# Kernel optimization log

Hardware: AMD Instinct MI355X
Metric: run time of the kernel (lower is better)

Reference implementation:

```python
import jax, jax.numpy as jnp
import numpy as np

N_NODES = 50000
N_EDGES = 800000
IN_DIM = 128
HIDDEN = 32
HEADS = 4
OUT_DIM = 40
NEG_SLOPE = 0.2


def _segment_softmax(logits, seg, num_segments):
    # logits: [E, H], seg: [E] destination node ids
    m = jax.ops.segment_max(logits, seg, num_segments=num_segments)  # [N, H]
    e = jnp.exp(logits - m[seg])
    s = jax.ops.segment_sum(e, seg, num_segments=num_segments)  # [N, H]
    return e / s[seg]


def _gat_conv(x, src, dst, W, a_src, a_dst, b, heads, out_ch, concat):
    N = x.shape[0]
    h = (x @ W).reshape(N, heads, out_ch)  # [N, H, C]
    alpha_src = jnp.einsum('nhc,hc->nh', h, a_src)  # [N, H]
    alpha_dst = jnp.einsum('nhc,hc->nh', h, a_dst)  # [N, H]
    logits = jax.nn.leaky_relu(alpha_src[src] + alpha_dst[dst], NEG_SLOPE)  # [E, H]
    alpha = _segment_softmax(logits, dst, N)  # [E, H]
    msg = h[src] * alpha[:, :, None]  # [E, H, C]
    out = jax.ops.segment_sum(msg, dst, num_segments=N)  # [N, H, C]
    if concat:
        out = out.reshape(N, heads * out_ch)
    else:
        out = out.mean(axis=1)
    return out + b


def setup_inputs() -> dict:
    key = jax.random.key(0)
    ks = jax.random.split(key, 12)
    x = jax.random.normal(ks[0], (N_NODES, IN_DIM), dtype=jnp.float32)
    edge_index = jax.random.randint(ks[1], (2, N_EDGES), 0, N_NODES, dtype=jnp.int64 if jax.config.read('jax_enable_x64') else jnp.int32)
    s1 = 1.0 / np.sqrt(IN_DIM)
    W1 = jax.random.uniform(ks[2], (IN_DIM, HEADS * HIDDEN), jnp.float32, -s1, s1)
    att_src1 = jax.random.uniform(ks[3], (HEADS, HIDDEN), jnp.float32, -1, 1) / np.sqrt(HIDDEN)
    att_dst1 = jax.random.uniform(ks[4], (HEADS, HIDDEN), jnp.float32, -1, 1) / np.sqrt(HIDDEN)
    b1 = jnp.zeros((HEADS * HIDDEN,), jnp.float32)
    s2 = 1.0 / np.sqrt(HEADS * HIDDEN)
    W2 = jax.random.uniform(ks[5], (HEADS * HIDDEN, OUT_DIM), jnp.float32, -s2, s2)
    att_src2 = jax.random.uniform(ks[6], (1, OUT_DIM), jnp.float32, -1, 1) / np.sqrt(OUT_DIM)
    att_dst2 = jax.random.uniform(ks[7], (1, OUT_DIM), jnp.float32, -1, 1) / np.sqrt(OUT_DIM)
    b2 = jnp.zeros((OUT_DIM,), jnp.float32)
    return {
        'x': x, 'edge_index': edge_index,
        'W1': W1, 'att_src1': att_src1, 'att_dst1': att_dst1, 'b1': b1,
        'W2': W2, 'att_src2': att_src2, 'att_dst2': att_dst2, 'b2': b2,
    }


def reference(x, edge_index, W1, att_src1, att_dst1, b1, W2, att_src2, att_dst2, b2):
    N = x.shape[0]
    # PyG GATConv default add_self_loops=True
    loop = jnp.arange(N, dtype=edge_index.dtype)
    src = jnp.concatenate([edge_index[0], loop])
    dst = jnp.concatenate([edge_index[1], loop])
    # dropout(p=0.6) is identity in eval mode
    h = _gat_conv(x, src, dst, W1, att_src1, att_dst1, b1, HEADS, HIDDEN, concat=True)
    h = jax.nn.relu(h)
    out = _gat_conv(h, src, dst, W2, att_src2, att_dst2, b2, 1, OUT_DIM, concat=True)
    return out
```

## Files before the change

### kernel.cpp

```cpp
#include <hip/hip_runtime.h>
#include <hip/hip_bf16.h>
#include <math.h>

#define N_NODES 50000
#define N_EDGES 800000
#define E_TOT   850000
#define IN_DIM  128
#define HID     32
#define HEADS   4
#define D1      128
#define OUT_DIM 40
#define H2P     64
#define NEG_SLOPE 0.2f

#define SCAN_TILE 1024
#define SCAN_NB   ((N_NODES + SCAN_TILE - 1) / SCAN_TILE)
#define GEMM1_NB  ((N_NODES + 31) / 32)
#define CNT_NB    ((E_TOT + 255) / 256)

__global__ __launch_bounds__(256) void gemm1_count(
    const float* __restrict__ x, const float* __restrict__ W,
    const float* __restrict__ as_v, const float* __restrict__ ad_v,
    float* __restrict__ h1, float* __restrict__ asrc, float* __restrict__ adst,
    const int* __restrict__ ei, int* __restrict__ deg)
{
  __shared__ float xs[32][IN_DIM];
  const int t = threadIdx.x;
  if (blockIdx.x >= GEMM1_NB) {
    int e = (blockIdx.x - GEMM1_NB) * 256 + t;
    if (e < E_TOT) {
      int d = (e < N_EDGES) ? ei[N_EDGES + e] : e - N_EDGES;
      atomicAdd(deg + d, 1);
    }
    return;
  }
  const int nb = blockIdx.x * 32;
  for (int i = t; i < 32 * (IN_DIM / 4); i += 256) {
    int r = i >> 5, k4 = (i & 31) * 4;
    int n = nb + r;
    float4 v = (n < N_NODES) ? *reinterpret_cast<const float4*>(x + (size_t)n * IN_DIM + k4)
                             : make_float4(0.f, 0.f, 0.f, 0.f);
    *reinterpret_cast<float4*>(&xs[r][k4]) = v;
  }
  __syncthreads();
  const int ct = t & 31, col0 = ct * 4;
  const int rt = t >> 5, rbase = rt * 4;
  float acc[4][4];
#pragma unroll
  for (int r = 0; r < 4; ++r)
#pragma unroll
    for (int c = 0; c < 4; ++c) acc[r][c] = 0.f;

  for (int k = 0; k < IN_DIM; k += 4) {
    float4 xv[4];
#pragma unroll
    for (int r = 0; r < 4; ++r)
      xv[r] = *reinterpret_cast<const float4*>(&xs[rbase + r][k]);
    float4 wv[4];
#pragma unroll
    for (int kk = 0; kk < 4; ++kk)
      wv[kk] = *reinterpret_cast<const float4*>(W + (size_t)(k + kk) * D1 + col0);
#pragma unroll
    for (int r = 0; r < 4; ++r) {
      acc[r][0] += xv[r].x * wv[0].x + xv[r].y * wv[1].x + xv[r].z * wv[2].x + xv[r].w * wv[3].x;
      acc[r][1] += xv[r].x * wv[0].y + xv[r].y * wv[1].y + xv[r].z * wv[2].y + xv[r].w * wv[3].y;
      acc[r][2] += xv[r].x * wv[0].z + xv[r].y * wv[1].z + xv[r].z * wv[2].z + xv[r].w * wv[3].z;
      acc[r][3] += xv[r].x * wv[0].w + xv[r].y * wv[1].w + xv[r].z * wv[2].w + xv[r].w * wv[3].w;
    }
  }

  const int head = col0 >> 5;
  const int cc0  = col0 & 31;
  const float4 asv = *reinterpret_cast<const float4*>(as_v + head * HID + cc0);
  const float4 adv = *reinterpret_cast<const float4*>(ad_v + head * HID + cc0);
#pragma unroll
  for (int r = 0; r < 4; ++r) {
    int n = nb + rbase + r;
    bool ok = n < N_NODES;
    if (ok) {
      float4 o = make_float4(acc[r][0], acc[r][1], acc[r][2], acc[r][3]);
      *reinterpret_cast<float4*>(h1 + (size_t)n * D1 + col0) = o;
    }
    float cs = acc[r][0] * asv.x + acc[r][1] * asv.y + acc[r][2] * asv.z + acc[r][3] * asv.w;
    float cd = acc[r][0] * adv.x + acc[r][1] * adv.y + acc[r][2] * adv.z + acc[r][3] * adv.w;
#pragma unroll
    for (int off = 1; off < 8; off <<= 1) {
      cs += __shfl_xor(cs, off, 64);
      cd += __shfl_xor(cd, off, 64);
    }
    if ((ct & 7) == 0 && ok) {
      asrc[n * HEADS + head] = cs;
      adst[n * HEADS + head] = cd;
    }
  }
}

__global__ void zero_deg(int* __restrict__ deg)
{
  int i = blockIdx.x * blockDim.x + threadIdx.x;
  if (i < N_NODES) deg[i] = 0;
}

__global__ __launch_bounds__(256) void scan_p1(const int* __restrict__ deg,
                                               int* __restrict__ blocksum)
{
  int base = blockIdx.x * SCAN_TILE + threadIdx.x * 4;
  int s = 0;
#pragma unroll
  for (int i = 0; i < 4; ++i) {
    int idx = base + i;
    if (idx < N_NODES) s += deg[idx];
  }
#pragma unroll
  for (int off = 1; off < 64; off <<= 1) s += __shfl_xor(s, off, 64);
  __shared__ int ws[4];
  if ((threadIdx.x & 63) == 0) ws[threadIdx.x >> 6] = s;
  __syncthreads();
  if (threadIdx.x == 0) blocksum[blockIdx.x] = ws[0] + ws[1] + ws[2] + ws[3];
}

__global__ void scan_p2(const int* __restrict__ blocksum, int* __restrict__ blockoff,
                        int* __restrict__ row_off)
{
  int t = threadIdx.x;
  int v = (t < SCAN_NB) ? blocksum[t] : 0;
  int incl = v;
#pragma unroll
  for (int off = 1; off < 64; off <<= 1) {
    int u = __shfl_up(incl, off, 64);
    if (t >= off) incl += u;
  }
  if (t < SCAN_NB) blockoff[t] = incl - v;
  if (t == 0) row_off[N_NODES] = E_TOT;
}

__global__ __launch_bounds__(256) void scan_p3(const int* __restrict__ deg,
                                               const int* __restrict__ blockoff,
                                               int* __restrict__ row_off,
                                               int* __restrict__ cursor)
{
  const int t = threadIdx.x;
  const int lane = t & 63, wid = t >> 6;
  int base = blockIdx.x * SCAN_TILE + t * 4;
  int local[4]; int lsum = 0;
#pragma unroll
  for (int i = 0; i < 4; ++i) {
    int idx = base + i;
    local[i] = (idx < N_NODES) ? deg[idx] : 0;
    lsum += local[i];
  }
  int incl = lsum;
#pragma unroll
  for (int off = 1; off < 64; off <<= 1) {
    int u = __shfl_up(incl, off, 64);
    if (lane >= off) incl += u;
  }
  __shared__ int wtot[4];
  if (lane == 63) wtot[wid] = incl;
  __syncthreads();
  int wpre = 0;
  for (int w = 0; w < wid; ++w) wpre += wtot[w];
  int run = blockoff[blockIdx.x] + wpre + (incl - lsum);
#pragma unroll
  for (int i = 0; i < 4; ++i) {
    int idx = base + i;
    if (idx < N_NODES) { row_off[idx] = run; cursor[idx] = run; run += local[i]; }
  }
}

__global__ void scatter_csr(const int* __restrict__ ei, int* __restrict__ cursor,
                            int* __restrict__ csr_src)
{
  int e = blockIdx.x * blockDim.x + threadIdx.x;
  if (e >= E_TOT) return;
  int s, d;
  if (e < N_EDGES) { s = ei[e]; d = ei[N_EDGES + e]; }
  else             { s = d = e - N_EDGES; }
  int pos = atomicAdd(cursor + d, 1);
  csr_src[pos] = s;
}

__global__ __launch_bounds__(256) void agg1(
    const int* __restrict__ row_off, const int* __restrict__ csr_src,
    const float* __restrict__ asrc, const float* __restrict__ adst,
    const float* __restrict__ h1, const float* __restrict__ b1,
    float* __restrict__ lbuf, float* __restrict__ z)
{
  int n = blockIdx.x * 4 + (threadIdx.x >> 6);
  if (n >= N_NODES) return;
  const int lane = threadIdx.x & 63;
  const int start = row_off[n], end = row_off[n + 1];
  const int h = lane & 3;
  const float adst_h = adst[n * HEADS + h];
  float vmax = -1e30f;
  for (int i = start + (lane >> 2); i < end; i += 16)
    vmax = fmaxf(vmax, asrc[csr_src[i] * HEADS + h]);
#pragma unroll
  for (int off = 4; off < 64; off <<= 1)
    vmax = fmaxf(vmax, __shfl_xor(vmax, off, 64));
  float v = vmax + adst_h;
  const float mle = v > 0.f ? v : NEG_SLOPE * v;
  float ssum = 0.f;
  for (int i = start + (lane >> 2); i < end; i += 16) {
    float tv = asrc[csr_src[i] * HEADS + h] + adst_h;
    float le = tv > 0.f ? tv : NEG_SLOPE * tv;
    float e = __expf(le - mle);
    lbuf[(size_t)i * 4 + h] = e;
    ssum += e;
  }
#pragma unroll
  for (int off = 4; off < 64; off <<= 1)
    ssum += __shfl_xor(ssum, off, 64);
  const int hh = lane >> 4;
  const float inv = 1.f / __shfl(ssum, hh, 64);
  float2 acc = make_float2(0.f, 0.f);
  int i = start;
  for (; i + 4 <= end; i += 4) {
    int s0 = csr_src[i], s1 = csr_src[i + 1], s2 = csr_src[i + 2], s3 = csr_src[i + 3];
    float c0 = lbuf[(size_t)(i    ) * 4 + hh];
    float c1 = lbuf[(size_t)(i + 1) * 4 + hh];
    float c2 = lbuf[(size_t)(i + 2) * 4 + hh];
    float c3 = lbuf[(size_t)(i + 3) * 4 + hh];
    float2 v0 = *reinterpret_cast<const float2*>(h1 + (size_t)s0 * D1 + 2 * lane);
    float2 v1 = *reinterpret_cast<const float2*>(h1 + (size_t)s1 * D1 + 2 * lane);
    float2 v2 = *reinterpret_cast<const float2*>(h1 + (size_t)s2 * D1 + 2 * lane);
    float2 v3 = *reinterpret_cast<const float2*>(h1 + (size_t)s3 * D1 + 2 * lane);
    acc.x += c0 * v0.x + c1 * v1.x + c2 * v2.x + c3 * v3.x;
    acc.y += c0 * v0.y + c1 * v1.y + c2 * v2.y + c3 * v3.y;
  }
  for (; i < end; ++i) {
    int s = csr_src[i];
    float c = lbuf[(size_t)i * 4 + hh];
    float2 hv = *reinterpret_cast<const float2*>(h1 + (size_t)s * D1 + 2 * lane);
    acc.x += c * hv.x;
    acc.y += c * hv.y;
  }
  float2 bb = *reinterpret_cast<const float2*>(b1 + 2 * lane);
  float r0 = acc.x * inv + bb.x;
  float r1 = acc.y * inv + bb.y;
  float2 o = make_float2(r0 > 0.f ? r0 : 0.f, r1 > 0.f ? r1 : 0.f);
  *reinterpret_cast<float2*>(z + (size_t)n * D1 + 2 * lane) = o;
}

__global__ __launch_bounds__(256) void gemm2(
    const float* __restrict__ z, const float* __restrict__ W2,
    const float* __restrict__ as2, const float* __restrict__ ad2,
    float* __restrict__ h2p, float* __restrict__ asrc2, float* __restrict__ adst2)
{
  __shared__ float zs[32][IN_DIM];
  const int nb = blockIdx.x * 32;
  const int t  = threadIdx.x;
  for (int i = t; i < 32 * (IN_DIM / 4); i += 256) {
    int r = i >> 5, k4 = (i & 31) * 4;
    int n = nb + r;
    float4 v = (n < N_NODES) ? *reinterpret_cast<const float4*>(z + (size_t)n * IN_DIM + k4)
                             : make_float4(0.f, 0.f, 0.f, 0.f);
    *reinterpret_cast<float4*>(&zs[r][k4]) = v;
  }
  __syncthreads();
  const int col = t & 63;
  const int rbase = (t >> 6) * 8;
  const bool valid = col < OUT_DIM;
  const int colc = valid ? col : (OUT_DIM - 1);
  float acc[8];
#pragma unroll
  for (int r = 0; r < 8; ++r) acc[r] = 0.f;
  for (int k = 0; k < IN_DIM; ++k) {
    float w = W2[k * OUT_DIM + colc];
#pragma unroll
    for (int r = 0; r < 8; ++r) acc[r] += zs[rbase + r][k] * w;
  }
  const float a_s = valid ? as2[col] : 0.f;
  const float a_d = valid ? ad2[col] : 0.f;
#pragma unroll
  for (int r = 0; r < 8; ++r) {
    int n = nb + rbase + r;
    float cs = acc[r] * a_s, cd = acc[r] * a_d;
#pragma unroll
    for (int off = 32; off >= 1; off >>= 1) {
      cs += __shfl_xor(cs, off, 64);
      cd += __shfl_xor(cd, off, 64);
    }
    if (n < N_NODES) {
      if (valid) h2p[(size_t)n * H2P + col] = acc[r];
      if (col == 0) { asrc2[n] = cs; adst2[n] = cd; }
    }
  }
}

__global__ __launch_bounds__(256) void agg2(
    const int* __restrict__ row_off, const int* __restrict__ csr_src,
    const float* __restrict__ asrc, const float* __restrict__ adst,
    const float* __restrict__ h2p, const float* __restrict__ b2,
    float* __restrict__ lbuf, float* __restrict__ out)
{
  int n = blockIdx.x * 4 + (threadIdx.x >> 6);
  if (n >= N_NODES) return;
  const int lane = threadIdx.x & 63;
  const int start = row_off[n], end = row_off[n + 1];
  const float adstn = adst[n];
  float vmax = -1e30f;
  for (int i = start + lane; i < end; i += 64)
    vmax = fmaxf(vmax, asrc[csr_src[i]]);
#pragma unroll
  for (int off = 1; off < 64; off <<= 1)
    vmax = fmaxf(vmax, __shfl_xor(vmax, off, 64));
  float v = vmax + adstn;
  const float mle = v > 0.f ? v : NEG_SLOPE * v;
  float ssum = 0.f;
  for (int i = start + lane; i < end; i += 64) {
    float t = asrc[csr_src[i]] + adstn;
    float le = t > 0.f ? t : NEG_SLOPE * t;
    float e = __expf(le - mle);
    lbuf[i] = e;
    ssum += e;
  }
#pragma unroll
  for (int off = 1; off < 64; off <<= 1)
    ssum += __shfl_xor(ssum, off, 64);
  const float inv = 1.f / ssum;
  if (lane < OUT_DIM) {
    float acc = 0.f;
    int i = start;
    for (; i + 4 <= end; i += 4) {
      int s0 = csr_src[i], s1 = csr_src[i + 1], s2 = csr_src[i + 2], s3 = csr_src[i + 3];
      float c0 = lbuf[i], c1 = lbuf[i + 1], c2 = lbuf[i + 2], c3 = lbuf[i + 3];
      acc += c0 * h2p[(size_t)s0 * H2P + lane]
           + c1 * h2p[(size_t)s1 * H2P + lane]
           + c2 * h2p[(size_t)s2 * H2P + lane]
           + c3 * h2p[(size_t)s3 * H2P + lane];
    }
    for (; i < end; ++i)
      acc += lbuf[i] * h2p[(size_t)csr_src[i] * H2P + lane];
    out[(size_t)n * OUT_DIM + lane] = acc * inv + b2[lane];
  }
}

extern "C" void kernel_launch(void* const* d_in, const int* in_sizes, int n_in,
                              void* d_out, int out_size, void* d_ws, size_t ws_size,
                              hipStream_t stream)
{
  const float* x    = (const float*)d_in[0];
  const int*   ei   = (const int*)  d_in[1];
  const float* W1   = (const float*)d_in[2];
  const float* as1  = (const float*)d_in[3];
  const float* ad1  = (const float*)d_in[4];
  const float* b1   = (const float*)d_in[5];
  const float* W2   = (const float*)d_in[6];
  const float* as2  = (const float*)d_in[7];
  const float* ad2  = (const float*)d_in[8];
  const float* b2   = (const float*)d_in[9];
  float* out = (float*)d_out;

  float* ws = (float*)d_ws;
  float* h1    = ws +  0;
  float* h2p   = ws +  0;
  float* z     = ws +  6400000;
  float* asrc1 = ws + 12800000;
  float* adst1 = ws + 13000000;
  float* asrc2 = ws + 13200000;
  float* adst2 = ws + 13250000;
  int* deg     = (int*)(ws + 13300000);
  int* row_off = (int*)(ws + 13350000);
  int* cursor  = (int*)(ws + 13410000);
  int* csr_src = (int*)(ws + 13460000);
  int* blocksum= (int*)(ws + 14320000);
  int* blockoff= (int*)(ws + 14320100);
  float* lbuf  = ws + 14400000;

  const int B = 256;
  zero_deg<<<(N_NODES + B - 1) / B, B, 0, stream>>>(deg);
  gemm1_count<<<GEMM1_NB + CNT_NB, B, 0, stream>>>(x, W1, as1, ad1, h1, asrc1, adst1, ei, deg);
  scan_p1<<<SCAN_NB, B, 0, stream>>>(deg, blocksum);
  scan_p2<<<1, 64, 0, stream>>>(blocksum, blockoff, row_off);
  scan_p3<<<SCAN_NB, B, 0, stream>>>(deg, blockoff, row_off, cursor);
  scatter_csr<<<(E_TOT + B - 1) / B, B, 0, stream>>>(ei, cursor, csr_src);
  agg1<<<(N_NODES + 3) / 4, B, 0, stream>>>(row_off, csr_src, asrc1, adst1, h1, b1, lbuf, z);
  gemm2<<<(N_NODES + 31) / 32, B, 0, stream>>>(z, W2, as2, ad2, h2p, asrc2, adst2);
  agg2<<<(N_NODES + 3) / 4, B, 0, stream>>>(row_off, csr_src, asrc2, adst2, h2p, b2, lbuf, out);
}
```

Baseline: 366.2 us.

## Stage GEMM weights in shared memory with larger row tiles

gemm1 now processes 64 rows per block (8 per thread) and streams W through a double-buffered shared-memory tile, prefetching the next 8 rows of W into registers during compute. Previously every thread read W straight from global memory. gemm2 now loads a transposed, padded copy of W2 into shared memory so each thread can read float4 weights along k instead of scalar global loads. This cuts global and cache traffic for the weights, at the cost of more shared memory, more registers, and an extra barrier per k-step in gemm1. The GEMMs are only part of a larger pipeline dominated by edge gathers, so the overall effect is bounded.

```diff
diff --git a/kernel.cpp b/kernel.cpp
--- a/kernel.cpp
+++ b/kernel.cpp
@@ -15,8 +15,10 @@
 
 #define SCAN_TILE 1024
 #define SCAN_NB   ((N_NODES + SCAN_TILE - 1) / SCAN_TILE)
-#define GEMM1_NB  ((N_NODES + 31) / 32)
+#define G1_ROWS   64
+#define GEMM1_NB  ((N_NODES + G1_ROWS - 1) / G1_ROWS)
 #define CNT_NB    ((E_TOT + 255) / 256)
+#define W2T_LD    132
 
 __global__ __launch_bounds__(256) void gemm1_count(
     const float* __restrict__ x, const float* __restrict__ W,
@@ -24,7 +26,8 @@
     float* __restrict__ h1, float* __restrict__ asrc, float* __restrict__ adst,
     const int* __restrict__ ei, int* __restrict__ deg)
 {
-  __shared__ float xs[32][IN_DIM];
+  __shared__ float xs[G1_ROWS][IN_DIM];
+  __shared__ float wbuf[2][8 * D1];
   const int t = threadIdx.x;
   if (blockIdx.x >= GEMM1_NB) {
     int e = (blockIdx.x - GEMM1_NB) * 256 + t;
@@ -34,39 +37,53 @@
     }
     return;
   }
-  const int nb = blockIdx.x * 32;
-  for (int i = t; i < 32 * (IN_DIM / 4); i += 256) {
+  const int nb = blockIdx.x * G1_ROWS;
+  for (int i = t; i < G1_ROWS * (IN_DIM / 4); i += 256) {
     int r = i >> 5, k4 = (i & 31) * 4;
     int n = nb + r;
     float4 v = (n < N_NODES) ? *reinterpret_cast<const float4*>(x + (size_t)n * IN_DIM + k4)
                              : make_float4(0.f, 0.f, 0.f, 0.f);
     *reinterpret_cast<float4*>(&xs[r][k4]) = v;
   }
+  float4 wreg = *reinterpret_cast<const float4*>(W + t * 4);
+  *reinterpret_cast<float4*>(&wbuf[0][t * 4]) = wreg;
   __syncthreads();
+
   const int ct = t & 31, col0 = ct * 4;
-  const int rt = t >> 5, rbase = rt * 4;
-  float acc[4][4];
-#pragma unroll
-  for (int r = 0; r < 4; ++r)
+  const int rt = t >> 5;
+  float acc[8][4];
+#pragma unroll
+  for (int r = 0; r < 8; ++r)
 #pragma unroll
     for (int c = 0; c < 4; ++c) acc[r][c] = 0.f;
 
-  for (int k = 0; k < IN_DIM; k += 4) {
-    float4 xv[4];
-#pragma unroll
-    for (int r = 0; r < 4; ++r)
-      xv[r] = *reinterpret_cast<const float4*>(&xs[rbase + r][k]);
-    float4 wv[4];
-#pragma unroll
-    for (int kk = 0; kk < 4; ++kk)
-      wv[kk] = *reinterpret_cast<const float4*>(W + (size_t)(k + kk) * D1 + col0);
-#pragma unroll
-    for (int r = 0; r < 4; ++r) {
-      acc[r][0] += xv[r].x * wv[0].x + xv[r].y * wv[1].x + xv[r].z * wv[2].x + xv[r].w * wv[3].x;
-      acc[r][1] += xv[r].x * wv[0].y + xv[r].y * wv[1].y + xv[r].z * wv[2].y + xv[r].w * wv[3].y;
-      acc[r][2] += xv[r].x * wv[0].z + xv[r].y * wv[1].z + xv[r].z * wv[2].z + xv[r].w * wv[3].z;
-      acc[r][3] += xv[r].x * wv[0].w + xv[r].y * wv[1].w + xv[r].z * wv[2].w + xv[r].w * wv[3].w;
-    }
+  const int NK8 = IN_DIM / 8;
+  for (int k8 = 0; k8 < NK8; ++k8) {
+    const int cur = k8 & 1;
+    if (k8 + 1 < NK8)
+      wreg = *reinterpret_cast<const float4*>(W + (size_t)(k8 + 1) * 8 * D1 + t * 4);
+#pragma unroll
+    for (int half = 0; half < 2; ++half) {
+      const int kb = k8 * 8 + half * 4;
+      float4 xv[8];
+#pragma unroll
+      for (int r = 0; r < 8; ++r)
+        xv[r] = *reinterpret_cast<const float4*>(&xs[rt * 8 + r][kb]);
+      float4 wv[4];
+#pragma unroll
+      for (int kk = 0; kk < 4; ++kk)
+        wv[kk] = *reinterpret_cast<const float4*>(&wbuf[cur][(half * 4 + kk) * D1 + col0]);
+#pragma unroll
+      for (int r = 0; r < 8; ++r) {
+        acc[r][0] += xv[r].x * wv[0].x + xv[r].y * wv[1].x + xv[r].z * wv[2].x + xv[r].w * wv[3].x;
+        acc[r][1] += xv[r].x * wv[0].y + xv[r].y * wv[1].y + xv[r].z * wv[2].y + xv[r].w * wv[3].y;
+        acc[r][2] += xv[r].x * wv[0].z + xv[r].y * wv[1].z + xv[r].z * wv[2].z + xv[r].w * wv[3].z;
+        acc[r][3] += xv[r].x * wv[0].w + xv[r].y * wv[1].w + xv[r].z * wv[2].w + xv[r].w * wv[3].w;
+      }
+    }
+    if (k8 + 1 < NK8)
+      *reinterpret_cast<float4*>(&wbuf[cur ^ 1][t * 4]) = wreg;
+    __syncthreads();
   }
 
   const int head = col0 >> 5;
@@ -74,8 +91,8 @@
   const float4 asv = *reinterpret_cast<const float4*>(as_v + head * HID + cc0);
   const float4 adv = *reinterpret_cast<const float4*>(ad_v + head * HID + cc0);
 #pragma unroll
-  for (int r = 0; r < 4; ++r) {
-    int n = nb + rbase + r;
+  for (int r = 0; r < 8; ++r) {
+    int n = nb + rt * 8 + r;
     bool ok = n < N_NODES;
     if (ok) {
       float4 o = make_float4(acc[r][0], acc[r][1], acc[r][2], acc[r][3]);
@@ -248,6 +265,7 @@
     float* __restrict__ h2p, float* __restrict__ asrc2, float* __restrict__ adst2)
 {
   __shared__ float zs[32][IN_DIM];
+  __shared__ float w2t[OUT_DIM][W2T_LD];
   const int nb = blockIdx.x * 32;
   const int t  = threadIdx.x;
   for (int i = t; i < 32 * (IN_DIM / 4); i += 256) {
@@ -257,6 +275,10 @@
                              : make_float4(0.f, 0.f, 0.f, 0.f);
     *reinterpret_cast<float4*>(&zs[r][k4]) = v;
   }
+  for (int i = t; i < IN_DIM * OUT_DIM; i += 256) {
+    int k = i / OUT_DIM, c = i - k * OUT_DIM;
+    w2t[c][k] = W2[i];
+  }
   __syncthreads();
   const int col = t & 63;
   const int rbase = (t >> 6) * 8;
@@ -265,10 +287,15 @@
   float acc[8];
 #pragma unroll
   for (int r = 0; r < 8; ++r) acc[r] = 0.f;
-  for (int k = 0; k < IN_DIM; ++k) {
-    float w = W2[k * OUT_DIM + colc];
-#pragma unroll
-    for (int r = 0; r < 8; ++r) acc[r] += zs[rbase + r][k] * w;
+  for (int k = 0; k < IN_DIM; k += 4) {
+    float4 wv = *reinterpret_cast<const float4*>(&w2t[colc][k]);
+    float4 xv[8];
+#pragma unroll
+    for (int r = 0; r < 8; ++r)
+      xv[r] = *reinterpret_cast<const float4*>(&zs[rbase + r][k]);
+#pragma unroll
+    for (int r = 0; r < 8; ++r)
+      acc[r] += xv[r].x * wv.x + xv[r].y * wv.y + xv[r].z * wv.z + xv[r].w * wv.w;
   }
   const float a_s = valid ? as2[col] : 0.f;
   const float a_d = valid ? ad2[col] : 0.f;
```

After: 350.7 us. 1.04x faster.
